# Kernel tuning notes

Hardware: AMD Instinct MI355X
Metric: run time of the kernel (lower is better)

Reference implementation:

```python
import jax, jax.numpy as jnp
import numpy as np

B, C, R, Cc = 16384, 30, 7, 7

def setup_inputs() -> dict:
    key = jax.random.key(0)
    k1, k2, k3 = jax.random.split(key, 3)
    pred = jax.random.uniform(k1, (B, C, R, Cc), dtype=jnp.float32)
    label = jax.random.uniform(k2, (B, C, R, Cc), dtype=jnp.float32)
    obj = (jax.random.uniform(k3, (B, R, Cc)) > 0.7).astype(jnp.float32)
    label = label.at[:, 4].set(obj)
    return {"pred": pred, "label": label}

def _boxes(t, cols, rows, nrow, ncol, off):
    # t: [b,30,r,c]; channels off..off+3 are (x,y,w,h) relative to cell
    x, y, w, h = t[:, off], t[:, off + 1], t[:, off + 2], t[:, off + 3]
    cx = (x + cols) / ncol
    cy = (y + rows) / nrow
    return cx - w / 2, cy - h / 2, cx + w / 2, cy + h / 2

def _iou(a, b):
    ax1, ay1, ax2, ay2 = a
    bx1, by1, bx2, by2 = b
    iw = jnp.maximum(jnp.minimum(ax2, bx2) - jnp.maximum(ax1, bx1), 0.0)
    ih = jnp.maximum(jnp.minimum(ay2, by2) - jnp.maximum(ay1, by1), 0.0)
    inter = iw * ih
    area_a = (ax2 - ax1) * (ay2 - ay1)
    area_b = (bx2 - bx1) * (by2 - by1)
    return inter / (area_a + area_b - inter + 1e-10)

def reference(pred, label):
    b_size = pred.shape[0]
    nrow, ncol = pred.shape[-2], pred.shape[-1]
    cols = jnp.arange(ncol, dtype=pred.dtype)[None, None, :]  # [1,1,c]
    rows = jnp.arange(nrow, dtype=pred.dtype)[None, :, None]  # [1,r,1]

    bbox1 = _boxes(pred, cols, rows, nrow, ncol, 0)
    bbox2 = _boxes(pred, cols, rows, nrow, ncol, 5)
    lbox = _boxes(label, cols, rows, nrow, ncol, 0)
    iou1 = _iou(bbox1, lbox)  # [b,r,c]
    iou2 = _iou(bbox2, lbox)
    choose1 = iou1 >= iou2

    # coord loss candidates (sum over the 2 xy channels / 2 wh channels)
    coord1 = 5.0 * jnp.sum((pred[:, 0:2] - label[:, 0:2]) ** 2, axis=1) \
           + jnp.sum((jnp.sqrt(pred[:, 2:4]) - jnp.sqrt(label[:, 2:4])) ** 2, axis=1)
    coord2 = 5.0 * jnp.sum((pred[:, 5:7] - label[:, 5:7]) ** 2, axis=1) \
           + jnp.sum((jnp.sqrt(pred[:, 7:9]) - jnp.sqrt(label[:, 7:9])) ** 2, axis=1)

    obj1 = (pred[:, 4] - iou1) ** 2
    obj2 = (pred[:, 9] - iou2) ** 2

    coord = jnp.where(choose1, coord1, coord2)
    obj_conf = jnp.where(choose1, obj1, obj2)
    noobj_conf_obj = 0.5 * jnp.where(choose1, obj2, obj1)
    class_l = jnp.sum((pred[:, 10:] - label[:, 10:]) ** 2, axis=1)

    obj_cell = coord + obj_conf + noobj_conf_obj + class_l
    # note: original sums the two confidences THEN squares (faithful to source)
    noobj_cell = 0.5 * (pred[:, 4] + pred[:, 9]) ** 2

    is_obj = label[:, 4] == 1.0
    per_cell = jnp.where(is_obj, obj_cell, noobj_cell)
    return jnp.sum(per_cell) / b_size
```

## Files before the change

kernel.cpp:

```cpp
#include <hip/hip_runtime.h>


typedef float v2f __attribute__((ext_vector_type(2)));

#define NBATCH 16384
#define RECF 1470
#define BLOCK 256
#define GRID (NBATCH / 4)

__device__ __forceinline__ float sq(float x) { return x * x; }

__device__ __forceinline__ float block_reduce(float v, float* smem, int tid) {
#pragma unroll
    for (int off = 32; off > 0; off >>= 1) v += __shfl_down(v, off, 64);
    const int lane = tid & 63, wave = tid >> 6;
    if (lane == 0) smem[wave] = v;
    __syncthreads();
    return smem[0] + smem[1] + smem[2] + smem[3];
}

__global__ __launch_bounds__(BLOCK) void k_fused(const float* __restrict__ pred,
                                                 const float* __restrict__ label,
                                                 float* __restrict__ partials) {
    __shared__ float lds[4][960];
    __shared__ float smem[4];
    const int tid = threadIdx.x, lane = tid & 63, wv = tid >> 6;
    const int rec = blockIdx.x * 4 + wv;
    float* ldsw = &lds[wv][0];
    v2f* wp2 = (v2f*)ldsw;
    v2f* wl2 = (v2f*)(ldsw + 496);

    const v2f* gp = (const v2f*)(pred + (size_t)rec * RECF);
    const v2f* gl = (const v2f*)(label + (size_t)rec * RECF);

    v2f sp[4], sl[4];
#pragma unroll
    for (int i = 0; i < 4; ++i) {
        int idx = i * 64 + lane;
        sp[i] = (idx < 245) ? gp[idx] : (v2f){0.0f, 0.0f};
        sl[i] = (idx < 221) ? gl[idx] : (v2f){0.0f, 0.0f};
    }
    v2f cpv[8], clv[8];
#pragma unroll
    for (int i = 0; i < 8; ++i) {
        int k = i * 64 + lane;
        if (k < 490) {
            cpv[i] = gp[245 + k];
            clv[i] = gl[245 + k];
        } else {
            cpv[i] = (v2f){0.0f, 0.0f};
            clv[i] = (v2f){0.0f, 0.0f};
        }
    }
    float w49 = (lane < 49) ? ((const float*)gl)[196 + lane] : 0.0f;

#pragma unroll
    for (int i = 0; i < 4; ++i) {
        int idx = i * 64 + lane;
        if (idx < 245) wp2[idx] = sp[i];
        if (idx < 221) wl2[idx] = sl[i];
    }

    float acc = 0.0f;
    int c = (2 * lane) % 49;
#pragma unroll
    for (int i = 0; i < 8; ++i) {
        float w0 = __shfl(w49, c, 64);
        int cn = (c == 48) ? 0 : c + 1;
        float w1 = __shfl(w49, cn, 64);
        float d0 = cpv[i].x - clv[i].x, d1 = cpv[i].y - clv[i].y;
        acc += w0 * d0 * d0 + w1 * d1 * d1;
        c += 30; if (c >= 49) c -= 49;
    }

    asm volatile("s_waitcnt lgkmcnt(0)" ::: "memory");
    if (lane < 49) {
        const int rr = lane / 7, cc = lane - rr * 7;
        const float fr = (float)rr, fcl = (float)cc;
        const float inv7 = 1.0f / 7.0f;

        float p[10], l[9];
#pragma unroll
        for (int ch = 0; ch < 10; ++ch) p[ch] = ldsw[ch * 49 + lane];
#pragma unroll
        for (int ch = 0; ch < 9; ++ch) l[ch] = ldsw[496 + ch * 49 + lane];

        float lcx = (l[0] + fcl) * inv7;
        float lcy = (l[1] + fr) * inv7;
        float lhw = l[2] * 0.5f, lhh = l[3] * 0.5f;
        float lx1 = lcx - lhw, ly1 = lcy - lhh;
        float lx2 = lcx + lhw, ly2 = lcy + lhh;
        float larea = (lx2 - lx1) * (ly2 - ly1);

        float cx1 = (p[0] + fcl) * inv7, cy1 = (p[1] + fr) * inv7;
        float x11 = cx1 - p[2] * 0.5f, y11 = cy1 - p[3] * 0.5f;
        float x12 = cx1 + p[2] * 0.5f, y12 = cy1 + p[3] * 0.5f;
        float iw1 = fmaxf(fminf(x12, lx2) - fmaxf(x11, lx1), 0.0f);
        float ih1 = fmaxf(fminf(y12, ly2) - fmaxf(y11, ly1), 0.0f);
        float int1 = iw1 * ih1;
        float a1 = (x12 - x11) * (y12 - y11);
        float iou1 = int1 / (a1 + larea - int1 + 1e-10f);

        float cx2 = (p[5] + fcl) * inv7, cy2 = (p[6] + fr) * inv7;
        float x21 = cx2 - p[7] * 0.5f, y21 = cy2 - p[8] * 0.5f;
        float x22 = cx2 + p[7] * 0.5f, y22 = cy2 + p[8] * 0.5f;
        float iw2 = fmaxf(fminf(x22, lx2) - fmaxf(x21, lx1), 0.0f);
        float ih2 = fmaxf(fminf(y22, ly2) - fmaxf(y21, ly1), 0.0f);
        float int2 = iw2 * ih2;
        float a2 = (x22 - x21) * (y22 - y21);
        float iou2 = int2 / (a2 + larea - int2 + 1e-10f);

        bool ch1 = iou1 >= iou2;

        float coord1 = 5.0f * (sq(p[0] - l[0]) + sq(p[1] - l[1]))
                     + sq(sqrtf(p[2]) - sqrtf(l[2])) + sq(sqrtf(p[3]) - sqrtf(l[3]));
        float coord2 = 5.0f * (sq(p[5] - l[5]) + sq(p[6] - l[6]))
                     + sq(sqrtf(p[7]) - sqrtf(l[7])) + sq(sqrtf(p[8]) - sqrtf(l[8]));
        float obj1 = sq(p[4] - iou1);
        float obj2 = sq(p[9] - iou2);

        float obj_cell = (ch1 ? coord1 : coord2)
                       + (ch1 ? obj1 : obj2)
                       + 0.5f * (ch1 ? obj2 : obj1);
        float noobj_cell = 0.5f * sq(p[4] + p[9]);

        acc += (l[4] == 1.0f) ? obj_cell : noobj_cell;
    }

    float s = block_reduce(acc, smem, tid);
    if (tid == 0) partials[blockIdx.x] = s;
}

__global__ __launch_bounds__(BLOCK) void k_reduce(const float* __restrict__ partials,
                                                  float* __restrict__ out) {
    __shared__ float smem[4];
    float s = 0.0f;
#pragma unroll
    for (int it = 0; it < GRID / BLOCK; ++it)
        s += partials[it * BLOCK + threadIdx.x];
    float t = block_reduce(s, smem, threadIdx.x);
    if (threadIdx.x == 0) out[0] = t * (1.0f / (float)NBATCH);
}

extern "C" void kernel_launch(void* const* d_in, const int* in_sizes, int n_in,
                              void* d_out, int out_size, void* d_ws, size_t ws_size,
                              hipStream_t stream) {
    const float* pred  = (const float*)d_in[0];
    const float* label = (const float*)d_in[1];
    float* out = (float*)d_out;
    float* part = (float*)d_ws;

    k_fused<<<GRID, BLOCK, 0, stream>>>(pred, label, part);
    k_reduce<<<1, BLOCK, 0, stream>>>(part, out);
}
```

Baseline: 204.3 us.

## Persistent waves with double-buffered async global-to-LDS record staging

```diff
diff --git a/kernel.cpp b/kernel.cpp
--- a/kernel.cpp
+++ b/kernel.cpp
@@ -4,11 +4,34 @@
 typedef float v2f __attribute__((ext_vector_type(2)));
 
 #define NBATCH 16384
-#define RECF 1470
-#define BLOCK 256
-#define GRID (NBATCH / 4)
+#define RECF   1470
+#define RECB   (RECF * 4)
+#define BLOCK  256
+#define NW     2048
+#define GRID   (NW / 4)
+#define RPW    (NBATCH / NW)
+#define STRIDEF 1536
+#define LIMITB  ((unsigned)NBATCH * RECB - 16u)
 
 __device__ __forceinline__ float sq(float x) { return x * x; }
+
+__device__ __forceinline__ void dma16(const float* g, float* l) {
+    __builtin_amdgcn_global_load_lds(
+        (const __attribute__((address_space(1))) void*)g,
+        (__attribute__((address_space(3))) void*)l, 16, 0, 0);
+}
+
+__device__ __forceinline__ void stage_rec(const char* gp, const char* gl,
+                                          float* lp, float* ll,
+                                          unsigned recOff, unsigned laneB) {
+#pragma unroll
+    for (int c = 0; c < 6; ++c) {
+        unsigned off = recOff + (unsigned)(c * 1024) + laneB;
+        if (c == 5) off = (off > LIMITB) ? LIMITB : off;
+        dma16((const float*)(gp + off), lp + c * 256);
+        dma16((const float*)(gl + off), ll + c * 256);
+    }
+}
 
 __device__ __forceinline__ float block_reduce(float v, float* smem, int tid) {
 #pragma unroll
@@ -22,109 +45,108 @@
 __global__ __launch_bounds__(BLOCK) void k_fused(const float* __restrict__ pred,
                                                  const float* __restrict__ label,
                                                  float* __restrict__ partials) {
-    __shared__ float lds[4][960];
+    __shared__ float lds[4][2][2][STRIDEF];
     __shared__ float smem[4];
     const int tid = threadIdx.x, lane = tid & 63, wv = tid >> 6;
-    const int rec = blockIdx.x * 4 + wv;
-    float* ldsw = &lds[wv][0];
-    v2f* wp2 = (v2f*)ldsw;
-    v2f* wl2 = (v2f*)(ldsw + 496);
+    const int gw = blockIdx.x * 4 + wv;
+    const unsigned laneB = (unsigned)lane * 16u;
+    const char* gp = (const char*)pred;
+    const char* gl = (const char*)label;
 
-    const v2f* gp = (const v2f*)(pred + (size_t)rec * RECF);
-    const v2f* gl = (const v2f*)(label + (size_t)rec * RECF);
+    float* bP0 = &lds[wv][0][0][0]; float* bL0 = &lds[wv][0][1][0];
+    float* bP1 = &lds[wv][1][0][0]; float* bL1 = &lds[wv][1][1][0];
 
-    v2f sp[4], sl[4];
-#pragma unroll
-    for (int i = 0; i < 4; ++i) {
-        int idx = i * 64 + lane;
-        sp[i] = (idx < 245) ? gp[idx] : (v2f){0.0f, 0.0f};
-        sl[i] = (idx < 221) ? gl[idx] : (v2f){0.0f, 0.0f};
-    }
-    v2f cpv[8], clv[8];
-#pragma unroll
-    for (int i = 0; i < 8; ++i) {
-        int k = i * 64 + lane;
-        if (k < 490) {
-            cpv[i] = gp[245 + k];
-            clv[i] = gl[245 + k];
-        } else {
-            cpv[i] = (v2f){0.0f, 0.0f};
-            clv[i] = (v2f){0.0f, 0.0f};
-        }
-    }
-    float w49 = (lane < 49) ? ((const float*)gl)[196 + lane] : 0.0f;
-
-#pragma unroll
-    for (int i = 0; i < 4; ++i) {
-        int idx = i * 64 + lane;
-        if (idx < 245) wp2[idx] = sp[i];
-        if (idx < 221) wl2[idx] = sl[i];
-    }
+    const int rr = lane / 7, cc = lane - rr * 7;
+    const float fr = (float)rr, fcl = (float)cc;
+    const float inv7 = 1.0f / 7.0f;
+    const int c0 = (2 * lane) % 49;
 
     float acc = 0.0f;
-    int c = (2 * lane) % 49;
+
+    stage_rec(gp, gl, bP0, bL0, (unsigned)gw * RECB, laneB);
+    __builtin_amdgcn_sched_barrier(0);
+
+    for (int t = 0; t < RPW; ++t) {
+        if (t + 1 < RPW) {
+            unsigned nOff = (unsigned)((t + 1) * NW + gw) * RECB;
+            float* nP = ((t + 1) & 1) ? bP1 : bP0;
+            float* nL = ((t + 1) & 1) ? bL1 : bL0;
+            stage_rec(gp, gl, nP, nL, nOff, laneB);
+            asm volatile("s_waitcnt vmcnt(12)" ::: "memory");
+        } else {
+            asm volatile("s_waitcnt vmcnt(0)" ::: "memory");
+        }
+        __builtin_amdgcn_sched_barrier(0);
+
+        const float* P = (t & 1) ? bP1 : bP0;
+        const float* L = (t & 1) ? bL1 : bL0;
+
+        float w49 = (lane < 49) ? L[196 + lane] : 0.0f;
+        int c = c0;
 #pragma unroll
-    for (int i = 0; i < 8; ++i) {
-        float w0 = __shfl(w49, c, 64);
-        int cn = (c == 48) ? 0 : c + 1;
-        float w1 = __shfl(w49, cn, 64);
-        float d0 = cpv[i].x - clv[i].x, d1 = cpv[i].y - clv[i].y;
-        acc += w0 * d0 * d0 + w1 * d1 * d1;
-        c += 30; if (c >= 49) c -= 49;
-    }
+        for (int i = 0; i < 8; ++i) {
+            int k = i * 64 + lane;
+            float d0 = 0.0f, d1 = 0.0f;
+            if (k < 490) {
+                v2f p2 = *(const v2f*)(P + 490 + 2 * k);
+                v2f l2 = *(const v2f*)(L + 490 + 2 * k);
+                d0 = p2.x - l2.x; d1 = p2.y - l2.y;
+            }
+            float w0 = __shfl(w49, c, 64);
+            int cn = (c == 48) ? 0 : c + 1;
+            float w1 = __shfl(w49, cn, 64);
+            acc += w0 * d0 * d0 + w1 * d1 * d1;
+            c += 30; if (c >= 49) c -= 49;
+        }
 
-    asm volatile("s_waitcnt lgkmcnt(0)" ::: "memory");
-    if (lane < 49) {
-        const int rr = lane / 7, cc = lane - rr * 7;
-        const float fr = (float)rr, fcl = (float)cc;
-        const float inv7 = 1.0f / 7.0f;
+        if (lane < 49) {
+            float p[10], l[9];
+#pragma unroll
+            for (int ch = 0; ch < 10; ++ch) p[ch] = P[ch * 49 + lane];
+#pragma unroll
+            for (int ch = 0; ch < 9; ++ch) l[ch] = L[ch * 49 + lane];
 
-        float p[10], l[9];
-#pragma unroll
-        for (int ch = 0; ch < 10; ++ch) p[ch] = ldsw[ch * 49 + lane];
-#pragma unroll
-        for (int ch = 0; ch < 9; ++ch) l[ch] = ldsw[496 + ch * 49 + lane];
+            float lcx = (l[0] + fcl) * inv7;
+            float lcy = (l[1] + fr) * inv7;
+            float lhw = l[2] * 0.5f, lhh = l[3] * 0.5f;
+            float lx1 = lcx - lhw, ly1 = lcy - lhh;
+            float lx2 = lcx + lhw, ly2 = lcy + lhh;
+            float larea = (lx2 - lx1) * (ly2 - ly1);
 
-        float lcx = (l[0] + fcl) * inv7;
-        float lcy = (l[1] + fr) * inv7;
-        float lhw = l[2] * 0.5f, lhh = l[3] * 0.5f;
-        float lx1 = lcx - lhw, ly1 = lcy - lhh;
-        float lx2 = lcx + lhw, ly2 = lcy + lhh;
-        float larea = (lx2 - lx1) * (ly2 - ly1);
+            float cx1 = (p[0] + fcl) * inv7, cy1 = (p[1] + fr) * inv7;
+            float x11 = cx1 - p[2] * 0.5f, y11 = cy1 - p[3] * 0.5f;
+            float x12 = cx1 + p[2] * 0.5f, y12 = cy1 + p[3] * 0.5f;
+            float iw1 = fmaxf(fminf(x12, lx2) - fmaxf(x11, lx1), 0.0f);
+            float ih1 = fmaxf(fminf(y12, ly2) - fmaxf(y11, ly1), 0.0f);
+            float int1 = iw1 * ih1;
+            float a1 = (x12 - x11) * (y12 - y11);
+            float iou1 = int1 / (a1 + larea - int1 + 1e-10f);
 
-        float cx1 = (p[0] + fcl) * inv7, cy1 = (p[1] + fr) * inv7;
-        float x11 = cx1 - p[2] * 0.5f, y11 = cy1 - p[3] * 0.5f;
-        float x12 = cx1 + p[2] * 0.5f, y12 = cy1 + p[3] * 0.5f;
-        float iw1 = fmaxf(fminf(x12, lx2) - fmaxf(x11, lx1), 0.0f);
-        float ih1 = fmaxf(fminf(y12, ly2) - fmaxf(y11, ly1), 0.0f);
-        float int1 = iw1 * ih1;
-        float a1 = (x12 - x11) * (y12 - y11);
-        float iou1 = int1 / (a1 + larea - int1 + 1e-10f);
+            float cx2 = (p[5] + fcl) * inv7, cy2 = (p[6] + fr) * inv7;
+            float x21 = cx2 - p[7] * 0.5f, y21 = cy2 - p[8] * 0.5f;
+            float x22 = cx2 + p[7] * 0.5f, y22 = cy2 + p[8] * 0.5f;
+            float iw2 = fmaxf(fminf(x22, lx2) - fmaxf(x21, lx1), 0.0f);
+            float ih2 = fmaxf(fminf(y22, ly2) - fmaxf(y21, ly1), 0.0f);
+            float int2 = iw2 * ih2;
+            float a2 = (x22 - x21) * (y22 - y21);
+            float iou2 = int2 / (a2 + larea - int2 + 1e-10f);
 
-        float cx2 = (p[5] + fcl) * inv7, cy2 = (p[6] + fr) * inv7;
-        float x21 = cx2 - p[7] * 0.5f, y21 = cy2 - p[8] * 0.5f;
-        float x22 = cx2 + p[7] * 0.5f, y22 = cy2 + p[8] * 0.5f;
-        float iw2 = fmaxf(fminf(x22, lx2) - fmaxf(x21, lx1), 0.0f);
-        float ih2 = fmaxf(fminf(y22, ly2) - fmaxf(y21, ly1), 0.0f);
-        float int2 = iw2 * ih2;
-        float a2 = (x22 - x21) * (y22 - y21);
-        float iou2 = int2 / (a2 + larea - int2 + 1e-10f);
+            bool ch1 = iou1 >= iou2;
 
-        bool ch1 = iou1 >= iou2;
+            float coord1 = 5.0f * (sq(p[0] - l[0]) + sq(p[1] - l[1]))
+                         + sq(sqrtf(p[2]) - sqrtf(l[2])) + sq(sqrtf(p[3]) - sqrtf(l[3]));
+            float coord2 = 5.0f * (sq(p[5] - l[5]) + sq(p[6] - l[6]))
+                         + sq(sqrtf(p[7]) - sqrtf(l[7])) + sq(sqrtf(p[8]) - sqrtf(l[8]));
+            float obj1 = sq(p[4] - iou1);
+            float obj2 = sq(p[9] - iou2);
 
-        float coord1 = 5.0f * (sq(p[0] - l[0]) + sq(p[1] - l[1]))
-                     + sq(sqrtf(p[2]) - sqrtf(l[2])) + sq(sqrtf(p[3]) - sqrtf(l[3]));
-        float coord2 = 5.0f * (sq(p[5] - l[5]) + sq(p[6] - l[6]))
-                     + sq(sqrtf(p[7]) - sqrtf(l[7])) + sq(sqrtf(p[8]) - sqrtf(l[8]));
-        float obj1 = sq(p[4] - iou1);
-        float obj2 = sq(p[9] - iou2);
+            float obj_cell = (ch1 ? coord1 : coord2)
+                           + (ch1 ? obj1 : obj2)
+                           + 0.5f * (ch1 ? obj2 : obj1);
+            float noobj_cell = 0.5f * sq(p[4] + p[9]);
 
-        float obj_cell = (ch1 ? coord1 : coord2)
-                       + (ch1 ? obj1 : obj2)
-                       + 0.5f * (ch1 ? obj2 : obj1);
-        float noobj_cell = 0.5f * sq(p[4] + p[9]);
-
-        acc += (l[4] == 1.0f) ? obj_cell : noobj_cell;
+            acc += (l[4] == 1.0f) ? obj_cell : noobj_cell;
+        }
     }
 
     float s = block_reduce(acc, smem, tid);
```

After: 207.7 us. Within noise of the previous version (+1.7%).

## Stage two records per block via 16-byte loads into LDS, split work across waves

Applied to the files above, without the earlier changes.

```diff
diff --git a/kernel.cpp b/kernel.cpp
--- a/kernel.cpp
+++ b/kernel.cpp
@@ -2,11 +2,13 @@
 
 
 typedef float v2f __attribute__((ext_vector_type(2)));
+typedef float v4f __attribute__((ext_vector_type(4)));
 
 #define NBATCH 16384
-#define RECF 1470
-#define BLOCK 256
-#define GRID (NBATCH / 4)
+#define RECF   1470
+#define BLOCK  256
+#define GRID   (NBATCH / 2)
+#define BLKF4  735
 
 __device__ __forceinline__ float sq(float x) { return x * x; }
 
@@ -22,68 +24,56 @@
 __global__ __launch_bounds__(BLOCK) void k_fused(const float* __restrict__ pred,
                                                  const float* __restrict__ label,
                                                  float* __restrict__ partials) {
-    __shared__ float lds[4][960];
+    __shared__ __align__(16) float lp[2 * RECF];
+    __shared__ __align__(16) float ll[2 * RECF];
     __shared__ float smem[4];
     const int tid = threadIdx.x, lane = tid & 63, wv = tid >> 6;
-    const int rec = blockIdx.x * 4 + wv;
-    float* ldsw = &lds[wv][0];
-    v2f* wp2 = (v2f*)ldsw;
-    v2f* wl2 = (v2f*)(ldsw + 496);
 
-    const v2f* gp = (const v2f*)(pred + (size_t)rec * RECF);
-    const v2f* gl = (const v2f*)(label + (size_t)rec * RECF);
+    const v4f* gp4 = (const v4f*)pred  + (size_t)blockIdx.x * BLKF4;
+    const v4f* gl4 = (const v4f*)label + (size_t)blockIdx.x * BLKF4;
 
-    v2f sp[4], sl[4];
+    const int i0 = tid, i1 = tid + 256, i2 = tid + 512;
+    const int i2c = (i2 < BLKF4) ? i2 : (BLKF4 - 1);
+    v4f p0 = gp4[i0];  v4f l0 = gl4[i0];
+    v4f p1 = gp4[i1];  v4f l1 = gl4[i1];
+    v4f p2 = gp4[i2c]; v4f l2 = gl4[i2c];
+    ((v4f*)lp)[i0] = p0; ((v4f*)ll)[i0] = l0;
+    ((v4f*)lp)[i1] = p1; ((v4f*)ll)[i1] = l1;
+    if (i2 < BLKF4) { ((v4f*)lp)[i2] = p2; ((v4f*)ll)[i2] = l2; }
+    __syncthreads();
+
+    const int rec = wv >> 1, sub = wv & 1;
+    const float* P = lp + rec * RECF;
+    const float* L = ll + rec * RECF;
+
+    float acc = 0.0f;
+
+    int c = (2 * (sub * 64 + lane)) % 49;
 #pragma unroll
     for (int i = 0; i < 4; ++i) {
-        int idx = i * 64 + lane;
-        sp[i] = (idx < 245) ? gp[idx] : (v2f){0.0f, 0.0f};
-        sl[i] = (idx < 221) ? gl[idx] : (v2f){0.0f, 0.0f};
-    }
-    v2f cpv[8], clv[8];
-#pragma unroll
-    for (int i = 0; i < 8; ++i) {
-        int k = i * 64 + lane;
+        int k = i * 128 + sub * 64 + lane;
         if (k < 490) {
-            cpv[i] = gp[245 + k];
-            clv[i] = gl[245 + k];
-        } else {
-            cpv[i] = (v2f){0.0f, 0.0f};
-            clv[i] = (v2f){0.0f, 0.0f};
+            v2f pp = *(const v2f*)(P + 490 + 2 * k);
+            v2f lq = *(const v2f*)(L + 490 + 2 * k);
+            float w0 = L[196 + c];
+            int cn = (c == 48) ? 0 : c + 1;
+            float w1 = L[196 + cn];
+            float d0 = pp.x - lq.x, d1 = pp.y - lq.y;
+            acc += w0 * d0 * d0 + w1 * d1 * d1;
         }
-    }
-    float w49 = (lane < 49) ? ((const float*)gl)[196 + lane] : 0.0f;
-
-#pragma unroll
-    for (int i = 0; i < 4; ++i) {
-        int idx = i * 64 + lane;
-        if (idx < 245) wp2[idx] = sp[i];
-        if (idx < 221) wl2[idx] = sl[i];
+        c += 11; if (c >= 49) c -= 49;
     }
 
-    float acc = 0.0f;
-    int c = (2 * lane) % 49;
-#pragma unroll
-    for (int i = 0; i < 8; ++i) {
-        float w0 = __shfl(w49, c, 64);
-        int cn = (c == 48) ? 0 : c + 1;
-        float w1 = __shfl(w49, cn, 64);
-        float d0 = cpv[i].x - clv[i].x, d1 = cpv[i].y - clv[i].y;
-        acc += w0 * d0 * d0 + w1 * d1 * d1;
-        c += 30; if (c >= 49) c -= 49;
-    }
-
-    asm volatile("s_waitcnt lgkmcnt(0)" ::: "memory");
-    if (lane < 49) {
+    if (sub == 1 && lane < 49) {
         const int rr = lane / 7, cc = lane - rr * 7;
         const float fr = (float)rr, fcl = (float)cc;
         const float inv7 = 1.0f / 7.0f;
 
         float p[10], l[9];
 #pragma unroll
-        for (int ch = 0; ch < 10; ++ch) p[ch] = ldsw[ch * 49 + lane];
+        for (int ch = 0; ch < 10; ++ch) p[ch] = P[ch * 49 + lane];
 #pragma unroll
-        for (int ch = 0; ch < 9; ++ch) l[ch] = ldsw[496 + ch * 49 + lane];
+        for (int ch = 0; ch < 9; ++ch) l[ch] = L[ch * 49 + lane];
 
         float lcx = (l[0] + fcl) * inv7;
         float lcy = (l[1] + fr) * inv7;
```

Measured after the change: 204.9 us. No clear change (+0.3%).
